# Kernel optimization log

Hardware: AMD Instinct MI355X
Metric: run time of the kernel (lower is better)

## Reference

```python
import jax, jax.numpy as jnp
import numpy as np

N, C, E, NUM_ID, NUM_LABELS = 50000, 128, 1600000, 2048, 7


def setup_inputs() -> dict:
    key = jax.random.key(0)
    k_x, k_r, k_c, k_id, k_lab, k_w, k_wid = jax.random.split(key, 7)
    x = jax.random.normal(k_x, (N, C), dtype=jnp.float32)
    row = jax.random.randint(k_r, (E,), 0, N)
    col = jax.random.randint(k_c, (E,), 0, N)
    # remove accidental self-loops so the 'add remaining self loops' step
    # (append all N self loops) matches PyG's add_remaining_self_loops exactly
    col = jnp.where(col == row, (col + 1) % N, col)
    edge_index = jnp.stack([row, col]).astype(jnp.int64)
    idx = jax.random.randint(k_id, (NUM_ID,), 0, N).astype(jnp.int64)
    node_label = jax.random.randint(k_lab, (N,), 0, 8).astype(jnp.int64)
    # glorot init
    s = jnp.sqrt(6.0 / (C + C)).astype(jnp.float32)
    weight = jax.random.uniform(k_w, (C, C), minval=-s, maxval=s, dtype=jnp.float32)
    weight_id = jax.random.uniform(k_wid, (NUM_LABELS, C, C), minval=-s, maxval=s, dtype=jnp.float32)
    return {"x": x, "edge_index": edge_index, "id": idx, "node_label": node_label,
            "weight": weight, "weight_id": weight_id}


def reference(x, edge_index, id, node_label, weight, weight_id):
    n = x.shape[0]
    row, col = edge_index[0], edge_index[1]
    # ego-center update: x[id] += x[id] @ W (index_add handles duplicate ids)
    x = x.at[id].add(x[id] @ weight)
    # label-grouped gather-matmul-scatter: ox = x + sum_i mask_i * (x @ W_i)
    ox = x
    for i in range(NUM_LABELS):
        mask = (node_label == i + 1)
        ox = ox + jnp.where(mask[:, None], x @ weight_id[i], jnp.zeros((), x.dtype))
    # GCN symmetric normalization with self loops (fill_value = 1.0)
    loop = jnp.arange(n)
    row_f = jnp.concatenate([row, loop])
    col_f = jnp.concatenate([col, loop])
    ew = jnp.ones((row_f.shape[0],), dtype=x.dtype)
    deg = jax.ops.segment_sum(ew, row_f, num_segments=n)
    dinv = jnp.where(deg > 0, deg ** -0.5, jnp.zeros((), x.dtype))
    norm = dinv[row_f] * ew * dinv[col_f]
    # message = norm * x_j (source row), aggregated by sum at target col
    out = jax.ops.segment_sum(norm[:, None] * ox[row_f], col_f, num_segments=n)
    return out
```

## Files before the change

kernel.cpp:

```cpp
#include <hip/hip_runtime.h>
#include <hip/hip_bf16.h>

typedef unsigned int   u32;
typedef unsigned short u16;
typedef unsigned char  u8;
typedef float f32x2 __attribute__((ext_vector_type(2)));
typedef float f32x4 __attribute__((ext_vector_type(4)));

#define N_NODES 50000
#define C_DIM   128
#define E_EDGES 1600000
#define NUM_IDX 2048

#define CPB 256
#define NB  196
#define CAP 9216
#define CHK 4096
#define NP  391
#define PT  512
#define GB  8

__global__ void label_hist_kernel(const int* __restrict__ label, int* __restrict__ labCnt,
                                  const int* __restrict__ id, int* __restrict__ cnt,
                                  int* __restrict__ colCursor, int* __restrict__ rowCursor) {
    __shared__ int h[8];
    if (threadIdx.x < 8) h[threadIdx.x] = 0;
    __syncthreads();
    int n = blockIdx.x * 256 + threadIdx.x;
    if (n < N_NODES) atomicAdd(&h[label[n]], 1);
    if (n < NUM_IDX) atomicAdd(&cnt[id[n]], 1);
    if (threadIdx.x == 0) {
        colCursor[blockIdx.x] = blockIdx.x * CAP;
        rowCursor[blockIdx.x] = blockIdx.x * CAP;
    }
    __syncthreads();
    if (threadIdx.x < 8 && h[threadIdx.x] > 0) atomicAdd(&labCnt[threadIdx.x], h[threadIdx.x]);
}

__global__ void label_base_kernel(const int* __restrict__ labCnt, int* __restrict__ labCur) {
    if (threadIdx.x == 0) {
        int run = 0;
        for (int i = 0; i < 8; ++i) { labCur[i] = run; run += labCnt[i]; }
    }
}

__global__ void partition_kernel(const int* __restrict__ row, const int* __restrict__ col,
                                 int* __restrict__ colCursor, int* __restrict__ rowCursor,
                                 u32* __restrict__ S, u8* __restrict__ Sr) {
    __shared__ int hc[NB], hr[NB], bc[NB], br[NB];
    int p = blockIdx.x;
    for (int i = threadIdx.x; i < NB; i += PT) { hc[i] = 0; hr[i] = 0; }
    __syncthreads();
    int e0 = p * CHK, e1 = min(e0 + CHK, E_EDGES);
    for (int e = e0 + threadIdx.x; e < e1; e += PT) {
        atomicAdd(&hc[col[e] >> 8], 1);
        atomicAdd(&hr[row[e] >> 8], 1);
    }
    __syncthreads();
    for (int i = threadIdx.x; i < NB; i += PT) {
        bc[i] = (hc[i] > 0) ? atomicAdd(&colCursor[i], hc[i]) : 0;
        br[i] = (hr[i] > 0) ? atomicAdd(&rowCursor[i], hr[i]) : 0;
    }
    __syncthreads();
    for (int e = e0 + threadIdx.x; e < e1; e += PT) {
        int r = row[e], c = col[e];
        int pc = atomicAdd(&bc[c >> 8], 1);
        S[pc] = ((u32)r << 8) | (u32)(c & 255);
        int pr = atomicAdd(&br[r >> 8], 1);
        Sr[pr] = (u8)(r & 255);
    }
}

__global__ void label_fill_kernel(const int* __restrict__ label, int* __restrict__ labCur,
                                  int* __restrict__ nodeByLabel) {
    __shared__ int h[8], base[8], c2[8];
    int t = threadIdx.x;
    if (t < 8) { h[t] = 0; c2[t] = 0; }
    __syncthreads();
    int n = blockIdx.x * 256 + t;
    int l = 0;
    if (n < N_NODES) { l = label[n]; atomicAdd(&h[l], 1); }
    __syncthreads();
    if (t < 8 && h[t] > 0) base[t] = atomicAdd(&labCur[t], h[t]);
    __syncthreads();
    if (n < N_NODES) {
        int pos = base[l] + atomicAdd(&c2[l], 1);
        nodeByLabel[pos] = n;
    }
}

__global__ void csr_deg_kernel(const u32* __restrict__ S, const u8* __restrict__ Sr,
                               const int* __restrict__ colCursor, const int* __restrict__ rowCursor,
                               int* __restrict__ s_beg, int* __restrict__ s_end,
                               u16* __restrict__ srcrow, float* __restrict__ dinv) {
    __shared__ int h[CPB], cur[CPB], sc[CPB];
    int t = threadIdx.x;
    if (blockIdx.x >= NB) {
        int b = blockIdx.x - NB;
        if (t < CPB) h[t] = 0;
        __syncthreads();
        int e0 = b * CAP, e1 = rowCursor[b];
        for (int e = e0 + t; e < e1; e += PT) atomicAdd(&h[Sr[e]], 1);
        __syncthreads();
        if (t < CPB) {
            int n = b * CPB + t;
            if (n < N_NODES) dinv[n] = rsqrtf((float)(h[t] + 1));
        }
        return;
    }
    int b = blockIdx.x;
    if (t < CPB) h[t] = 0;
    __syncthreads();
    int e0 = b * CAP, e1 = colCursor[b];
    for (int e = e0 + t; e < e1; e += PT) atomicAdd(&h[S[e] & 255u], 1);
    __syncthreads();
    if (t < CPB) sc[t] = h[t];
    __syncthreads();
    for (int off = 1; off < CPB; off <<= 1) {
        int v = 0, a = 0;
        if (t < CPB) { v = sc[t]; a = (t >= off) ? sc[t - off] : 0; }
        __syncthreads();
        if (t < CPB) sc[t] = v + a;
        __syncthreads();
    }
    if (t < CPB) {
        int base = (t == 0) ? 0 : sc[t - 1];
        int gcol = b * CPB + t;
        if (gcol < N_NODES) {
            s_beg[gcol] = e0 + base;
            s_end[gcol] = e0 + base + h[t];
        }
        cur[t] = base;
    }
    __syncthreads();
    for (int e = e0 + t; e < e1; e += PT) {
        u32 v = S[e];
        int pos = atomicAdd(&cur[v & 255u], 1);
        srcrow[e0 + pos] = (u16)(v >> 8);
    }
}

__global__ void node_msg_kernel(const float* __restrict__ x,
                                const int* __restrict__ cnt,
                                const int* __restrict__ label,
                                const float* __restrict__ dinv,
                                const float* __restrict__ W,
                                const float* __restrict__ Wid,
                                const int* __restrict__ nodeByLabel,
                                __hip_bfloat16* __restrict__ msgb) {
    __shared__ float xs[GB][C_DIM];
    __shared__ int nid[GB], lab[GB], cc[GB];
    int t = threadIdx.x;
    if (t < GB) {
        int n = nodeByLabel[blockIdx.x * GB + t];
        nid[t] = n; lab[t] = label[n]; cc[t] = cnt[n];
    }
    __syncthreads();
    #pragma unroll
    for (int g = 0; g < GB; ++g)
        xs[g][t] = __builtin_nontemporal_load(x + (size_t)nid[g] * C_DIM + t);
    __syncthreads();
    for (int g = 0; g < GB; ++g) {
        int c = cc[g];
        if (c > 0) {
            float acc = 0.f;
            #pragma unroll 8
            for (int k = 0; k < C_DIM; ++k) acc += xs[g][k] * W[k * C_DIM + t];
            __syncthreads();
            xs[g][t] += (float)c * acc;
            __syncthreads();
        }
    }
    float res[GB];
    #pragma unroll
    for (int g = 0; g < GB; ++g) res[g] = xs[g][t];
    if (lab[0] == lab[GB - 1]) {
        int L = lab[0];
        if (L > 0) {
            const float* Wl = Wid + (size_t)(L - 1) * C_DIM * C_DIM;
            float acc[GB];
            #pragma unroll
            for (int g = 0; g < GB; ++g) acc[g] = 0.f;
            for (int k = 0; k < C_DIM; ++k) {
                float w = Wl[k * C_DIM + t];
                #pragma unroll
                for (int g = 0; g < GB; ++g) acc[g] += xs[g][k] * w;
            }
            #pragma unroll
            for (int g = 0; g < GB; ++g) res[g] += acc[g];
        }
    } else {
        for (int g = 0; g < GB; ++g) {
            int L = lab[g];
            if (L > 0) {
                const float* Wl = Wid + (size_t)(L - 1) * C_DIM * C_DIM;
                float acc = 0.f;
                #pragma unroll 8
                for (int k = 0; k < C_DIM; ++k) acc += xs[g][k] * Wl[k * C_DIM + t];
                res[g] += acc;
            }
        }
    }
    #pragma unroll
    for (int g = 0; g < GB; ++g) {
        int n = nid[g];
        msgb[(size_t)n * C_DIM + t] = __float2bfloat16(dinv[n] * res[g]);
    }
}

__global__ void gather_kernel(const int* __restrict__ s_beg, const int* __restrict__ s_end,
                              const u16* __restrict__ srcrow,
                              const float* __restrict__ dinv,
                              const u32* __restrict__ m32,
                              float* __restrict__ out) {
    int wid  = threadIdx.x >> 6;
    int lane = threadIdx.x & 63;
    int g = lane >> 4;
    int q = lane & 15;
    int c = blockIdx.x * 4 + wid;
    int e0 = s_beg[c], e1 = s_end[c];
    const uint4* m4 = (const uint4*)m32;

    float a0[4], a1[4];
    #pragma unroll
    for (int k = 0; k < 4; ++k) { a0[k] = 0.f; a1[k] = 0.f; }

    #define ACC4(U)                                                          \
        a0[0] += __uint_as_float((U).x << 16); a1[0] += __uint_as_float((U).x & 0xffff0000u); \
        a0[1] += __uint_as_float((U).y << 16); a1[1] += __uint_as_float((U).y & 0xffff0000u); \
        a0[2] += __uint_as_float((U).z << 16); a1[2] += __uint_as_float((U).z & 0xffff0000u); \
        a0[3] += __uint_as_float((U).w << 16); a1[3] += __uint_as_float((U).w & 0xffff0000u);

    int e = e0;
    for (; e + 8 <= e1; e += 8) {
        u32 r0 = srcrow[e + g];
        u32 r1 = srcrow[e + 4 + g];
        uint4 u0 = m4[r0 * 16u + (u32)q];
        uint4 u1 = m4[r1 * 16u + (u32)q];
        ACC4(u0);
        ACC4(u1);
    }
    if (e + 4 <= e1) {
        u32 r0 = srcrow[e + g];
        uint4 u0 = m4[r0 * 16u + (u32)q];
        ACC4(u0);
        e += 4;
    }
    if (g == 0) {
        uint4 us = m4[(u32)c * 16u + (u32)q];
        ACC4(us);
        for (; e < e1; ++e) {
            u32 r = srcrow[e];
            uint4 u = m4[r * 16u + (u32)q];
            ACC4(u);
        }
    }
    #undef ACC4

    #pragma unroll
    for (int k = 0; k < 4; ++k) {
        a0[k] += __shfl_xor(a0[k], 16);
        a0[k] += __shfl_xor(a0[k], 32);
        a1[k] += __shfl_xor(a1[k], 16);
        a1[k] += __shfl_xor(a1[k], 32);
    }

    if (lane < 16) {
        float di = dinv[c];
        f32x4 o0, o1;
        o0.x = di * a0[0]; o0.y = di * a1[0]; o0.z = di * a0[1]; o0.w = di * a1[1];
        o1.x = di * a0[2]; o1.y = di * a1[2]; o1.z = di * a0[3]; o1.w = di * a1[3];
        f32x4* op = (f32x4*)(out + ((size_t)c << 7)) + (q << 1);
        __builtin_nontemporal_store(o0, op);
        __builtin_nontemporal_store(o1, op + 1);
    }
}

extern "C" void kernel_launch(void* const* d_in, const int* in_sizes, int n_in,
                              void* d_out, int out_size, void* d_ws, size_t ws_size,
                              hipStream_t stream) {
    const float* x     = (const float*)d_in[0];
    const int*   edge  = (const int*)d_in[1];
    const int*   id    = (const int*)d_in[2];
    const int*   label = (const int*)d_in[3];
    const float* W     = (const float*)d_in[4];
    const float* Wid   = (const float*)d_in[5];
    float*       out   = (float*)d_out;

    const int* row = edge;
    const int* col = edge + E_EDGES;

    __hip_bfloat16* msgb = (__hip_bfloat16*)d_ws;
    u32* S           = (u32*)(msgb + (size_t)N_NODES * C_DIM);
    u16* srcrow      = (u16*)(S + (size_t)NB * CAP);
    u8*  Sr          = (u8*)(srcrow + (size_t)NB * CAP);
    int* s_beg       = (int*)(Sr + (size_t)NB * CAP);
    int* s_end       = s_beg + N_NODES;
    int* colCursor   = s_end + N_NODES;
    int* rowCursor   = colCursor + NB;
    int* nodeByLabel = rowCursor + NB;
    float* dinv      = (float*)(nodeByLabel + N_NODES);
    int* cnt         = (int*)(dinv + N_NODES);
    int* labCnt      = cnt + N_NODES;
    int* labCur      = labCnt + 8;

    hipMemsetAsync(cnt, 0, ((size_t)N_NODES + 16) * sizeof(int), stream);

    label_hist_kernel <<<196, 256, 0, stream>>>(label, labCnt, id, cnt, colCursor, rowCursor);
    label_base_kernel <<<1, 64, 0, stream>>>(labCnt, labCur);
    partition_kernel  <<<NP, PT, 0, stream>>>(row, col, colCursor, rowCursor, S, Sr);
    label_fill_kernel <<<196, 256, 0, stream>>>(label, labCur, nodeByLabel);
    csr_deg_kernel    <<<2 * NB, PT, 0, stream>>>(S, Sr, colCursor, rowCursor,
                                                  s_beg, s_end, srcrow, dinv);
    node_msg_kernel   <<<N_NODES / GB, C_DIM, 0, stream>>>(x, cnt, label, dinv, W, Wid,
                                                           nodeByLabel, msgb);
    gather_kernel     <<<N_NODES / 4, 256, 0, stream>>>(s_beg, s_end, srcrow, dinv,
                                                        (const u32*)msgb, out);
}
```

Baseline: 237.2 us.

## Build CSR with global atomic degree histogram, scan, and atomic scatter

Replaces the two-pass bucketed partition (256-node stripes with shared-memory histograms and staging buffers) with a direct CSR build. Global atomics compute per-node in/out degrees, a two-level scan produces row starts, and a global-atomic scatter writes source rows. This drops the intermediate S/Sr buffers and their second pass. In exchange it relies on 3.2M global atomics over 50k addresses and adds more small kernel launches.

```diff
diff --git a/kernel.cpp b/kernel.cpp
--- a/kernel.cpp
+++ b/kernel.cpp
@@ -12,63 +12,90 @@
 #define E_EDGES 1600000
 #define NUM_IDX 2048
 
-#define CPB 256
-#define NB  196
-#define CAP 9216
-#define CHK 4096
-#define NP  391
-#define PT  512
+#define NS  196
 #define GB  8
 
 __global__ void label_hist_kernel(const int* __restrict__ label, int* __restrict__ labCnt,
-                                  const int* __restrict__ id, int* __restrict__ cnt,
-                                  int* __restrict__ colCursor, int* __restrict__ rowCursor) {
+                                  const int* __restrict__ id, int* __restrict__ cnt) {
     __shared__ int h[8];
     if (threadIdx.x < 8) h[threadIdx.x] = 0;
     __syncthreads();
     int n = blockIdx.x * 256 + threadIdx.x;
     if (n < N_NODES) atomicAdd(&h[label[n]], 1);
     if (n < NUM_IDX) atomicAdd(&cnt[id[n]], 1);
-    if (threadIdx.x == 0) {
-        colCursor[blockIdx.x] = blockIdx.x * CAP;
-        rowCursor[blockIdx.x] = blockIdx.x * CAP;
-    }
     __syncthreads();
     if (threadIdx.x < 8 && h[threadIdx.x] > 0) atomicAdd(&labCnt[threadIdx.x], h[threadIdx.x]);
 }
 
-__global__ void label_base_kernel(const int* __restrict__ labCnt, int* __restrict__ labCur) {
-    if (threadIdx.x == 0) {
+__global__ void edge_hist_kernel(const int* __restrict__ row, const int* __restrict__ col,
+                                 int* __restrict__ rowDeg, int* __restrict__ colDeg) {
+    int i = blockIdx.x * blockDim.x + threadIdx.x;
+    int stride = gridDim.x * blockDim.x;
+    for (int e = i; e < E_EDGES; e += stride) {
+        atomicAdd(&colDeg[col[e]], 1);
+        atomicAdd(&rowDeg[row[e]], 1);
+    }
+}
+
+__global__ void stripe_kernel(const int* __restrict__ colDeg, const int* __restrict__ rowDeg,
+                              int* __restrict__ stripeSum, float* __restrict__ dinv) {
+    __shared__ int sh[256];
+    int t = threadIdx.x;
+    int n = blockIdx.x * 256 + t;
+    int v = (n < N_NODES) ? colDeg[n] : 0;
+    if (n < N_NODES) dinv[n] = rsqrtf((float)(rowDeg[n] + 1));
+    sh[t] = v;
+    __syncthreads();
+    for (int off = 128; off > 0; off >>= 1) {
+        if (t < off) sh[t] += sh[t + off];
+        __syncthreads();
+    }
+    if (t == 0) stripeSum[blockIdx.x] = sh[0];
+}
+
+__global__ void stripe_scan_kernel(const int* __restrict__ stripeSum, int* __restrict__ stripeBase,
+                                   const int* __restrict__ labCnt, int* __restrict__ labCur) {
+    __shared__ int sc[256];
+    int t = threadIdx.x;
+    int v = (t < NS) ? stripeSum[t] : 0;
+    sc[t] = v;
+    __syncthreads();
+    for (int off = 1; off < 256; off <<= 1) {
+        int s = sc[t];
+        int a = (t >= off) ? sc[t - off] : 0;
+        __syncthreads();
+        sc[t] = s + a;
+        __syncthreads();
+    }
+    if (t < NS) stripeBase[t] = sc[t] - v;
+    if (t == 0) {
         int run = 0;
         for (int i = 0; i < 8; ++i) { labCur[i] = run; run += labCnt[i]; }
     }
 }
 
-__global__ void partition_kernel(const int* __restrict__ row, const int* __restrict__ col,
-                                 int* __restrict__ colCursor, int* __restrict__ rowCursor,
-                                 u32* __restrict__ S, u8* __restrict__ Sr) {
-    __shared__ int hc[NB], hr[NB], bc[NB], br[NB];
-    int p = blockIdx.x;
-    for (int i = threadIdx.x; i < NB; i += PT) { hc[i] = 0; hr[i] = 0; }
-    __syncthreads();
-    int e0 = p * CHK, e1 = min(e0 + CHK, E_EDGES);
-    for (int e = e0 + threadIdx.x; e < e1; e += PT) {
-        atomicAdd(&hc[col[e] >> 8], 1);
-        atomicAdd(&hr[row[e] >> 8], 1);
-    }
-    __syncthreads();
-    for (int i = threadIdx.x; i < NB; i += PT) {
-        bc[i] = (hc[i] > 0) ? atomicAdd(&colCursor[i], hc[i]) : 0;
-        br[i] = (hr[i] > 0) ? atomicAdd(&rowCursor[i], hr[i]) : 0;
-    }
-    __syncthreads();
-    for (int e = e0 + threadIdx.x; e < e1; e += PT) {
-        int r = row[e], c = col[e];
-        int pc = atomicAdd(&bc[c >> 8], 1);
-        S[pc] = ((u32)r << 8) | (u32)(c & 255);
-        int pr = atomicAdd(&br[r >> 8], 1);
-        Sr[pr] = (u8)(r & 255);
-    }
+__global__ void node_scan_kernel(const int* __restrict__ colDeg, const int* __restrict__ stripeBase,
+                                 int* __restrict__ start, int* __restrict__ cur) {
+    __shared__ int sc[256];
+    int t = threadIdx.x;
+    int b = blockIdx.x;
+    int n = b * 256 + t;
+    int v = (n < N_NODES) ? colDeg[n] : 0;
+    sc[t] = v;
+    __syncthreads();
+    for (int off = 1; off < 256; off <<= 1) {
+        int s = sc[t];
+        int a = (t >= off) ? sc[t - off] : 0;
+        __syncthreads();
+        sc[t] = s + a;
+        __syncthreads();
+    }
+    if (n < N_NODES) {
+        int s = stripeBase[b] + sc[t] - v;
+        start[n] = s;
+        cur[n]   = s;
+    }
+    if (b == NS - 1 && t == 0) start[N_NODES] = E_EDGES;
 }
 
 __global__ void label_fill_kernel(const int* __restrict__ label, int* __restrict__ labCur,
@@ -89,54 +116,13 @@
     }
 }
 
-__global__ void csr_deg_kernel(const u32* __restrict__ S, const u8* __restrict__ Sr,
-                               const int* __restrict__ colCursor, const int* __restrict__ rowCursor,
-                               int* __restrict__ s_beg, int* __restrict__ s_end,
-                               u16* __restrict__ srcrow, float* __restrict__ dinv) {
-    __shared__ int h[CPB], cur[CPB], sc[CPB];
-    int t = threadIdx.x;
-    if (blockIdx.x >= NB) {
-        int b = blockIdx.x - NB;
-        if (t < CPB) h[t] = 0;
-        __syncthreads();
-        int e0 = b * CAP, e1 = rowCursor[b];
-        for (int e = e0 + t; e < e1; e += PT) atomicAdd(&h[Sr[e]], 1);
-        __syncthreads();
-        if (t < CPB) {
-            int n = b * CPB + t;
-            if (n < N_NODES) dinv[n] = rsqrtf((float)(h[t] + 1));
-        }
-        return;
-    }
-    int b = blockIdx.x;
-    if (t < CPB) h[t] = 0;
-    __syncthreads();
-    int e0 = b * CAP, e1 = colCursor[b];
-    for (int e = e0 + t; e < e1; e += PT) atomicAdd(&h[S[e] & 255u], 1);
-    __syncthreads();
-    if (t < CPB) sc[t] = h[t];
-    __syncthreads();
-    for (int off = 1; off < CPB; off <<= 1) {
-        int v = 0, a = 0;
-        if (t < CPB) { v = sc[t]; a = (t >= off) ? sc[t - off] : 0; }
-        __syncthreads();
-        if (t < CPB) sc[t] = v + a;
-        __syncthreads();
-    }
-    if (t < CPB) {
-        int base = (t == 0) ? 0 : sc[t - 1];
-        int gcol = b * CPB + t;
-        if (gcol < N_NODES) {
-            s_beg[gcol] = e0 + base;
-            s_end[gcol] = e0 + base + h[t];
-        }
-        cur[t] = base;
-    }
-    __syncthreads();
-    for (int e = e0 + t; e < e1; e += PT) {
-        u32 v = S[e];
-        int pos = atomicAdd(&cur[v & 255u], 1);
-        srcrow[e0 + pos] = (u16)(v >> 8);
+__global__ void scatter_kernel(const int* __restrict__ row, const int* __restrict__ col,
+                               int* __restrict__ cur, u16* __restrict__ srcrow) {
+    int i = blockIdx.x * blockDim.x + threadIdx.x;
+    int stride = gridDim.x * blockDim.x;
+    for (int e = i; e < E_EDGES; e += stride) {
+        int pos = atomicAdd(&cur[col[e]], 1);
+        srcrow[pos] = (u16)row[e];
     }
 }
 
@@ -208,7 +194,7 @@
     }
 }
 
-__global__ void gather_kernel(const int* __restrict__ s_beg, const int* __restrict__ s_end,
+__global__ void gather_kernel(const int* __restrict__ start,
                               const u16* __restrict__ srcrow,
                               const float* __restrict__ dinv,
                               const u32* __restrict__ m32,
@@ -218,7 +204,7 @@
     int g = lane >> 4;
     int q = lane & 15;
     int c = blockIdx.x * 4 + wid;
-    int e0 = s_beg[c], e1 = s_end[c];
+    int e0 = start[c], e1 = start[c + 1];
     const uint4* m4 = (const uint4*)m32;
 
     float a0[4], a1[4];
@@ -291,29 +277,30 @@
     const int* col = edge + E_EDGES;
 
     __hip_bfloat16* msgb = (__hip_bfloat16*)d_ws;
-    u32* S           = (u32*)(msgb + (size_t)N_NODES * C_DIM);
-    u16* srcrow      = (u16*)(S + (size_t)NB * CAP);
-    u8*  Sr          = (u8*)(srcrow + (size_t)NB * CAP);
-    int* s_beg       = (int*)(Sr + (size_t)NB * CAP);
-    int* s_end       = s_beg + N_NODES;
-    int* colCursor   = s_end + N_NODES;
-    int* rowCursor   = colCursor + NB;
-    int* nodeByLabel = rowCursor + NB;
+    u16* srcrow      = (u16*)(msgb + (size_t)N_NODES * C_DIM);
+    int* start       = (int*)(srcrow + E_EDGES);
+    int* cur         = start + (N_NODES + 1);
+    int* stripeSum   = cur + N_NODES;
+    int* stripeBase  = stripeSum + 256;
+    int* nodeByLabel = stripeBase + 256;
     float* dinv      = (float*)(nodeByLabel + N_NODES);
     int* cnt         = (int*)(dinv + N_NODES);
-    int* labCnt      = cnt + N_NODES;
+    int* colDeg      = cnt + N_NODES;
+    int* rowDeg      = colDeg + N_NODES;
+    int* labCnt      = rowDeg + N_NODES;
     int* labCur      = labCnt + 8;
 
-    hipMemsetAsync(cnt, 0, ((size_t)N_NODES + 16) * sizeof(int), stream);
-
-    label_hist_kernel <<<196, 256, 0, stream>>>(label, labCnt, id, cnt, colCursor, rowCursor);
-    label_base_kernel <<<1, 64, 0, stream>>>(labCnt, labCur);
-    partition_kernel  <<<NP, PT, 0, stream>>>(row, col, colCursor, rowCursor, S, Sr);
+    hipMemsetAsync(cnt, 0, ((size_t)3 * N_NODES + 16) * sizeof(int), stream);
+
+    label_hist_kernel <<<196, 256, 0, stream>>>(label, labCnt, id, cnt);
+    edge_hist_kernel  <<<2048, 256, 0, stream>>>(row, col, rowDeg, colDeg);
+    stripe_kernel     <<<NS, 256, 0, stream>>>(colDeg, rowDeg, stripeSum, dinv);
+    stripe_scan_kernel<<<1, 256, 0, stream>>>(stripeSum, stripeBase, labCnt, labCur);
+    node_scan_kernel  <<<NS, 256, 0, stream>>>(colDeg, stripeBase, start, cur);
     label_fill_kernel <<<196, 256, 0, stream>>>(label, labCur, nodeByLabel);
-    csr_deg_kernel    <<<2 * NB, PT, 0, stream>>>(S, Sr, colCursor, rowCursor,
-                                                  s_beg, s_end, srcrow, dinv);
+    scatter_kernel    <<<2048, 256, 0, stream>>>(row, col, cur, srcrow);
     node_msg_kernel   <<<N_NODES / GB, C_DIM, 0, stream>>>(x, cnt, label, dinv, W, Wid,
                                                            nodeByLabel, msgb);
-    gather_kernel     <<<N_NODES / 4, 256, 0, stream>>>(s_beg, s_end, srcrow, dinv,
+    gather_kernel     <<<N_NODES / 4, 256, 0, stream>>>(start, srcrow, dinv,
                                                         (const u32*)msgb, out);
 }
```

After: 442.4 us. 1.86x slower.
